# Performance work log

Hardware: AMD Instinct MI355X
Metric: run time of the kernel (lower is better)

The kernel has to match this reference:

```python
import jax, jax.numpy as jnp
import numpy as np

GROUPS = 8
EPS = 1e-5


def group_norm_dim1(x, gamma, beta):
    # Faithful to torch: GroupNorm treats dim 1 (height) as the channel axis.
    B, H, W, C = x.shape
    xg = x.reshape(B, GROUPS, H // GROUPS, W, C)
    mean = xg.mean(axis=(2, 3, 4), keepdims=True)
    var = xg.var(axis=(2, 3, 4), keepdims=True)
    xn = ((xg - mean) * jax.lax.rsqrt(var + EPS)).reshape(B, H, W, C)
    return xn * gamma[None, :, None, None] + beta[None, :, None, None]


def setup_inputs() -> dict:
    key = jax.random.key(0)
    ks = jax.random.split(key, 8)
    B, H, W, C = 4, 64, 64, 64  # height must equal units for GroupNorm to apply
    s = 1.0 / np.sqrt(C)
    return {
        "x": jax.random.normal(ks[0], (B, H, W, C), dtype=jnp.float32),
        "gamma": jnp.ones((C,), jnp.float32),
        "beta": jnp.zeros((C,), jnp.float32),
        "Wq": jax.random.normal(ks[1], (C, C), jnp.float32) * s,
        "bq": jnp.zeros((C,), jnp.float32),
        "Wk": jax.random.normal(ks[2], (C, C), jnp.float32) * s,
        "bk": jnp.zeros((C,), jnp.float32),
        "Wv": jax.random.normal(ks[3], (C, C), jnp.float32) * s,
        "bv": jnp.zeros((C,), jnp.float32),
        "Wo": jax.random.normal(ks[4], (C, C), jnp.float32) * s,
        "bo": jnp.zeros((C,), jnp.float32),
    }


def reference(x, gamma, beta, Wq, bq, Wk, bk, Wv, bv, Wo, bo):
    B, H, W, C = x.shape
    scale = C ** (-0.5)
    xn = group_norm_dim1(x, gamma, beta)
    q = xn @ Wq + bq
    k = xn @ Wk + bk
    v = xn @ Wv + bv
    # full spatial self-attention: scores [B, H, W, H*W]
    scores = jnp.einsum('bhwc,bijc->bhwij', q, k) * scale
    attn = jax.nn.softmax(scores.reshape(B, H, W, H * W), axis=-1)
    attn = attn.reshape(B, H, W, H, W)
    proj = jnp.einsum('bhwij,bijc->bhwc', attn, v)
    proj = proj @ Wo + bo
    return xn + proj
```

## Files before the change

### kernel.cpp

```cpp
#include <hip/hip_runtime.h>

typedef __bf16 bf16_t;
typedef bf16_t bf16x8 __attribute__((ext_vector_type(8)));
typedef bf16_t bf16x4 __attribute__((ext_vector_type(4)));
typedef short  short4v __attribute__((ext_vector_type(4)));
typedef float  f32x4  __attribute__((ext_vector_type(4)));

#define MFMA32(a, b, c) __builtin_amdgcn_mfma_f32_16x16x32_bf16(a, b, c, 0, 0, 0)
#define MFMA16(a, b, c) __builtin_amdgcn_mfma_f32_16x16x16bf16_1k(a, b, c, 0, 0, 0)

typedef __attribute__((address_space(3))) unsigned int       lds_u32;
typedef __attribute__((address_space(1))) const unsigned int glb_u32c;
#define DMA16(GP, LP) __builtin_amdgcn_global_load_lds((glb_u32c*)(const void*)(GP), \
                                                       (lds_u32*)(void*)(LP), 16, 0, 0)

__global__ __launch_bounds__(256) void gn1w_kernel(const float* __restrict__ x,
    float2* __restrict__ partials,
    const float* __restrict__ Wq, const float* __restrict__ Wk,
    const float* __restrict__ Wv, const float* __restrict__ Wo,
    bf16_t* __restrict__ Wt) {
  int blk = blockIdx.x, t = threadIdx.x;
  if (blk >= 256) {
    int idx = (blk - 256) * 256 + t;
    int wsel = idx >> 12, rem = idx & 4095;
    int c = rem >> 6, kk = rem & 63;
    const float* src = (wsel == 0) ? Wq : ((wsel == 1) ? Wk : ((wsel == 2) ? Wv : Wo));
    Wt[idx] = (bf16_t)src[kk * 64 + c];
    return;
  }
  const float4* x4 = (const float4*)x + (size_t)blk * 1024;
  float s = 0.f, sq = 0.f;
  #pragma unroll
  for (int u = 0; u < 4; ++u) {
    float4 v = x4[u * 256 + t];
    s  += v.x + v.y + v.z + v.w;
    sq += v.x * v.x + v.y * v.y + v.z * v.z + v.w * v.w;
  }
  for (int off = 32; off; off >>= 1) {
    s  += __shfl_down(s, off, 64);
    sq += __shfl_down(sq, off, 64);
  }
  __shared__ float2 ps[4];
  if ((t & 63) == 0) ps[t >> 6] = make_float2(s, sq);
  __syncthreads();
  if (t == 0) {
    float S = 0.f, Q = 0.f;
    #pragma unroll
    for (int i = 0; i < 4; ++i) { S += ps[i].x; Q += ps[i].y; }
    partials[blk] = make_float2(S, Q);
  }
}

__global__ __launch_bounds__(256) void gnqkv_kernel(
    const float* __restrict__ x, const float* __restrict__ gamma,
    const float* __restrict__ beta, const float2* __restrict__ parts,
    const bf16_t* __restrict__ Wt,
    const float* __restrict__ bq, const float* __restrict__ bk, const float* __restrict__ bv,
    bf16_t* __restrict__ xnb, bf16_t* __restrict__ qo, bf16_t* __restrict__ ko,
    bf16_t* __restrict__ vo) {
  __shared__ __align__(16) bf16_t xl[4096];
  int blk = blockIdx.x, t = threadIdx.x;
  int grp = blk >> 3;
  float S = 0.f, Q = 0.f;
  #pragma unroll
  for (int i = 0; i < 8; ++i) { float2 p = parts[grp * 8 + i]; S += p.x; Q += p.y; }
  float mean = S * (1.f / 32768.f);
  float rstd = rsqrtf(Q * (1.f / 32768.f) - mean * mean + 1e-5f);
  int h = blk & 63;
  float ga = gamma[h] * rstd;
  float be = beta[h] - mean * ga;
  {
    int r = t >> 2, col0 = (t & 3) * 16;
    const float4* x4 = (const float4*)(x + (size_t)blk * 4096 + r * 64 + col0);
    bf16x8 pk0, pk1;
    float4 v0 = x4[0], v1 = x4[1], v2 = x4[2], v3 = x4[3];
    pk0[0] = (bf16_t)(v0.x * ga + be); pk0[1] = (bf16_t)(v0.y * ga + be);
    pk0[2] = (bf16_t)(v0.z * ga + be); pk0[3] = (bf16_t)(v0.w * ga + be);
    pk0[4] = (bf16_t)(v1.x * ga + be); pk0[5] = (bf16_t)(v1.y * ga + be);
    pk0[6] = (bf16_t)(v1.z * ga + be); pk0[7] = (bf16_t)(v1.w * ga + be);
    pk1[0] = (bf16_t)(v2.x * ga + be); pk1[1] = (bf16_t)(v2.y * ga + be);
    pk1[2] = (bf16_t)(v2.z * ga + be); pk1[3] = (bf16_t)(v2.w * ga + be);
    pk1[4] = (bf16_t)(v3.x * ga + be); pk1[5] = (bf16_t)(v3.y * ga + be);
    pk1[6] = (bf16_t)(v3.z * ga + be); pk1[7] = (bf16_t)(v3.w * ga + be);
    *(bf16x8*)&xnb[(size_t)blk * 4096 + r * 64 + col0]     = pk0;
    *(bf16x8*)&xnb[(size_t)blk * 4096 + r * 64 + col0 + 8] = pk1;
    int sw = r & 7, j0 = (t & 3) * 2;
    *(bf16x8*)&xl[r * 64 + ((j0 ^ sw) << 3)]       = pk0;
    *(bf16x8*)&xl[r * 64 + (((j0 + 1) ^ sw) << 3)] = pk1;
  }
  __syncthreads();
  int w = t >> 6, lane = t & 63, quad = lane >> 4, l16 = lane & 15;
  int rl = w * 16 + l16, sw2 = rl & 7;
  bf16x8 a0 = *(const bf16x8*)&xl[rl * 64 + ((quad ^ sw2) << 3)];
  bf16x8 a1 = *(const bf16x8*)&xl[rl * 64 + (((quad + 4) ^ sw2) << 3)];
  int m0 = blk * 64 + w * 16;
  int bi = blk >> 6;
  int tile = blk & 63;
  size_t tbase = (size_t)bi * 262144 + (size_t)tile * 4096;
  f32x4 zero = {0.f, 0.f, 0.f, 0.f};
  const float QSCALE = 0.125f * 1.44269504088896340736f;
  #pragma unroll
  for (int outk = 0; outk < 3; ++outk) {
    const bf16_t* wt = Wt + outk * 4096;
    const float* bias = (outk == 0) ? bq : ((outk == 1) ? bk : bv);
    #pragma unroll
    for (int nt = 0; nt < 4; ++nt) {
      int col = nt * 16 + l16;
      bf16x8 b0 = *(const bf16x8*)&wt[col * 64 + quad * 8];
      bf16x8 b1 = *(const bf16x8*)&wt[col * 64 + 32 + quad * 8];
      f32x4 acc = MFMA32(a0, b0, zero);
      acc = MFMA32(a1, b1, acc);
      float bb = bias[col];
      if (outk == 0) {
        #pragma unroll
        for (int r = 0; r < 4; ++r) {
          int m = m0 + quad * 4 + r;
          qo[(size_t)m * 64 + col] = (bf16_t)((acc[r] + bb) * QSCALE);
        }
      } else if (outk == 1) {
        #pragma unroll
        for (int r = 0; r < 4; ++r) {
          int kk = (m0 & 63) + quad * 4 + r;
          ko[tbase + kk * 64 + ((((col >> 3) ^ (kk & 7)) << 3) | (col & 7))]
              = (bf16_t)(acc[r] + bb);
        }
      } else {
        bf16x4 pk;
        #pragma unroll
        for (int r = 0; r < 4; ++r) pk[r] = (bf16_t)(acc[r] + bb);
        int u = w * 4 + quad;
        *(bf16x4*)&vo[tbase + col * 64 + ((u ^ ((col & 7) << 1)) << 2)] = pk;
      }
    }
  }
}

__global__ __launch_bounds__(256, 2) void flash_kernel(
    const bf16_t* __restrict__ q, const bf16_t* __restrict__ k,
    const bf16_t* __restrict__ vp, bf16_t* __restrict__ Opb, float* __restrict__ ml) {
  __shared__ __align__(16) bf16_t Kb[2][8192];
  __shared__ __align__(16) bf16_t Vb[2][8192];
  int t = threadIdx.x;
  int w = t >> 6, lane = t & 63, quad = lane >> 4, l16 = lane & 15;
  int b = blockIdx.x, qb = blockIdx.y, sp = blockIdx.z;
  int q0 = qb * 128 + w * 32;

  bf16x8 qf[2][2];
  {
    const bf16_t* qp = q + ((size_t)b * 4096 + q0 + l16) * 64;
    #pragma unroll
    for (int qt = 0; qt < 2; ++qt)
      #pragma unroll
      for (int hh = 0; hh < 2; ++hh)
        qf[qt][hh] = *(const bf16x8*)&qp[qt * 1024 + hh * 32 + quad * 8];
  }
  f32x4 o[2][4];
  f32x4 zero = {0.f, 0.f, 0.f, 0.f};
  #pragma unroll
  for (int qt = 0; qt < 2; ++qt)
    #pragma unroll
    for (int ct = 0; ct < 4; ++ct) o[qt][ct] = zero;
  float rs[2] = {0.f, 0.f};

  const bf16_t* kimg = k  + (size_t)b * 262144 + (size_t)sp * 65536 + w * 2048 + lane * 8;
  const bf16_t* vimg = vp + (size_t)b * 262144 + (size_t)sp * 65536 + w * 2048 + lane * 8;

  #pragma unroll
  for (int i = 0; i < 4; ++i) {
    DMA16(kimg + i * 512, &Kb[0][w * 2048 + i * 512]);
    DMA16(vimg + i * 512, &Vb[0][w * 2048 + i * 512]);
  }
  __syncthreads();

  int swk = l16 & 7;
  int swv = (l16 & 7) << 1;

  for (int it = 0; it < 8; ++it) {
    int cur = it & 1;
    if (it < 7) {
      const bf16_t* kg = kimg + (it + 1) * 8192;
      const bf16_t* vg = vimg + (it + 1) * 8192;
      int nxt = cur ^ 1;
      #pragma unroll
      for (int i = 0; i < 4; ++i) {
        DMA16(kg + i * 512, &Kb[nxt][w * 2048 + i * 512]);
        DMA16(vg + i * 512, &Vb[nxt][w * 2048 + i * 512]);
      }
    }
    #pragma unroll
    for (int kt = 0; kt < 8; ++kt) {
      const bf16_t* Kh = &Kb[cur][(kt >> 2) * 4096];
      const bf16_t* Vh = &Vb[cur][(kt >> 2) * 4096];
      int krow = ((kt & 3) * 16 + l16) * 64;
      bf16x8 kf0 = *(const bf16x8*)&Kh[krow + ((quad ^ swk) << 3)];
      bf16x8 kf1 = *(const bf16x8*)&Kh[krow + (((quad + 4) ^ swk) << 3)];
      short4v va[4];
      #pragma unroll
      for (int ct = 0; ct < 4; ++ct)
        va[ct] = *(const short4v*)&Vh[(ct * 16 + l16) * 64 + ((((kt & 3) * 4 + quad) ^ swv) << 2)];
      #pragma unroll
      for (int qt = 0; qt < 2; ++qt) {
        f32x4 st = MFMA32(kf0, qf[qt][0], zero);
        st = MFMA32(kf1, qf[qt][1], st);
        bf16x4 pb;
        float psum = 0.f;
        #pragma unroll
        for (int r = 0; r < 4; ++r) {
          float p = __builtin_amdgcn_exp2f(st[r]);
          psum += p;
          pb[r] = (bf16_t)p;
        }
        rs[qt] += psum;
        short4v pshort = __builtin_bit_cast(short4v, pb);
        #pragma unroll
        for (int ct = 0; ct < 4; ++ct)
          o[qt][ct] = MFMA16(va[ct], pshort, o[qt][ct]);
      }
    }
    __syncthreads();
  }

  #pragma unroll
  for (int qt = 0; qt < 2; ++qt) {
    rs[qt] += __shfl_xor(rs[qt], 16, 64);
    rs[qt] += __shfl_xor(rs[qt], 32, 64);
  }
  size_t rbase = (size_t)sp * 16384 + (size_t)b * 4096 + q0;
  #pragma unroll
  for (int qt = 0; qt < 2; ++qt) {
    size_t row = rbase + qt * 16 + l16;
    if (quad == 0) ml[row] = rs[qt];
    #pragma unroll
    for (int ct = 0; ct < 4; ++ct) {
      bf16x4 pk;
      #pragma unroll
      for (int r = 0; r < 4; ++r) pk[r] = (bf16_t)o[qt][ct][r];
      *(bf16x4*)&Opb[row * 64 + ct * 16 + quad * 4] = pk;
    }
  }
}

__global__ __launch_bounds__(256) void proj_kernel(
    const bf16_t* __restrict__ Opb, const float* __restrict__ ml,
    const bf16_t* __restrict__ Wt, const float* __restrict__ bo,
    const bf16_t* __restrict__ xnb, float* __restrict__ out) {
  int t = threadIdx.x, w = t >> 6, lane = t & 63, quad = lane >> 4, l16 = lane & 15;
  int r0 = blockIdx.x * 64 + w * 16;
  float acc0[8], acc1[8];
  #pragma unroll
  for (int e = 0; e < 8; ++e) { acc0[e] = 0.f; acc1[e] = 0.f; }
  float lsum = 0.f;
  #pragma unroll
  for (int s = 0; s < 4; ++s) {
    size_t rr = (size_t)s * 16384 + r0 + l16;
    bf16x8 f0 = *(const bf16x8*)&Opb[rr * 64 + quad * 8];
    bf16x8 f1 = *(const bf16x8*)&Opb[rr * 64 + 32 + quad * 8];
    #pragma unroll
    for (int e = 0; e < 8; ++e) { acc0[e] += (float)f0[e]; acc1[e] += (float)f1[e]; }
    lsum += ml[rr];
  }
  float linv = 1.f / lsum;
  bf16x8 a0, a1;
  #pragma unroll
  for (int e = 0; e < 8; ++e) {
    a0[e] = (bf16_t)(acc0[e] * linv);
    a1[e] = (bf16_t)(acc1[e] * linv);
  }
  f32x4 zero = {0.f, 0.f, 0.f, 0.f};
  const bf16_t* wt = Wt + 3 * 4096;
  #pragma unroll
  for (int nt = 0; nt < 4; ++nt) {
    int col = nt * 16 + l16;
    bf16x8 b0 = *(const bf16x8*)&wt[col * 64 + quad * 8];
    bf16x8 b1 = *(const bf16x8*)&wt[col * 64 + 32 + quad * 8];
    f32x4 acc = MFMA32(a0, b0, zero);
    acc = MFMA32(a1, b1, acc);
    float bb = bo[col];
    #pragma unroll
    for (int r = 0; r < 4; ++r) {
      size_t m = (size_t)r0 + quad * 4 + r;
      out[m * 64 + col] = acc[r] + bb + (float)xnb[m * 64 + col];
    }
  }
}

extern "C" void kernel_launch(void* const* d_in, const int* in_sizes, int n_in,
                              void* d_out, int out_size, void* d_ws, size_t ws_size,
                              hipStream_t stream) {
  const float* x     = (const float*)d_in[0];
  const float* gamma = (const float*)d_in[1];
  const float* beta  = (const float*)d_in[2];
  const float* Wq    = (const float*)d_in[3];
  const float* bq    = (const float*)d_in[4];
  const float* Wk    = (const float*)d_in[5];
  const float* bk    = (const float*)d_in[6];
  const float* Wv    = (const float*)d_in[7];
  const float* bv    = (const float*)d_in[8];
  const float* Wo    = (const float*)d_in[9];
  const float* bo    = (const float*)d_in[10];
  float* out = (float*)d_out;

  char* ws = (char*)d_ws;
  bf16_t* xnb   = (bf16_t*)(ws + 0);
  bf16_t* qb    = (bf16_t*)(ws + (2u  << 20));
  bf16_t* kb    = (bf16_t*)(ws + (4u  << 20));
  bf16_t* vb    = (bf16_t*)(ws + (6u  << 20));
  bf16_t* Opb   = (bf16_t*)(ws + (8u  << 20));
  float*  ml    = (float*)(ws + (16u << 20));
  float2* parts = (float2*)(ws + (17u << 20));
  bf16_t* Wt    = (bf16_t*)(ws + (17u << 20) + 4096);

  hipLaunchKernelGGL(gn1w_kernel,  dim3(320),       dim3(256), 0, stream, x, parts, Wq, Wk, Wv, Wo, Wt);
  hipLaunchKernelGGL(gnqkv_kernel, dim3(256),       dim3(256), 0, stream, x, gamma, beta, parts, Wt, bq, bk, bv, xnb, qb, kb, vb);
  hipLaunchKernelGGL(flash_kernel, dim3(4, 32, 4),  dim3(256), 0, stream, qb, kb, vb, Opb, ml);
  hipLaunchKernelGGL(proj_kernel,  dim3(256),       dim3(256), 0, stream, Opb, ml, Wt, bo, xnb, out);
}
```

Before: 122.3 us.

## Use 16x16x32 MFMA for PV, widen query tile, double key splits

The PV product now uses the K=32 bf16 MFMA instead of the K=16 variant. Two key tiles are processed per step, and the V layout written by the QKV kernel is permuted so 8 contiguous bf16 can be loaded per lane. Each wave now handles 64 queries (256 per block), and the key range is split 8 ways instead of 4, so each block walks half the keys. The proj kernel reduces over 8 partials and the workspace offsets move to fit the larger partial buffer. The aim is fewer MFMA instructions and better reuse of K/V fragments, at the cost of more registers per thread and more partial-output traffic.

```diff
diff --git a/kernel.cpp b/kernel.cpp
--- a/kernel.cpp
+++ b/kernel.cpp
@@ -3,11 +3,9 @@
 typedef __bf16 bf16_t;
 typedef bf16_t bf16x8 __attribute__((ext_vector_type(8)));
 typedef bf16_t bf16x4 __attribute__((ext_vector_type(4)));
-typedef short  short4v __attribute__((ext_vector_type(4)));
 typedef float  f32x4  __attribute__((ext_vector_type(4)));
 
 #define MFMA32(a, b, c) __builtin_amdgcn_mfma_f32_16x16x32_bf16(a, b, c, 0, 0, 0)
-#define MFMA16(a, b, c) __builtin_amdgcn_mfma_f32_16x16x16bf16_1k(a, b, c, 0, 0, 0)
 
 typedef __attribute__((address_space(3))) unsigned int       lds_u32;
 typedef __attribute__((address_space(1))) const unsigned int glb_u32c;
@@ -128,7 +126,7 @@
         bf16x4 pk;
         #pragma unroll
         for (int r = 0; r < 4; ++r) pk[r] = (bf16_t)(acc[r] + bb);
-        int u = w * 4 + quad;
+        int u = (w >> 1) * 8 + quad * 2 + (w & 1);
         *(bf16x4*)&vo[tbase + col * 64 + ((u ^ ((col & 7) << 1)) << 2)] = pk;
       }
     }
@@ -143,27 +141,27 @@
   int t = threadIdx.x;
   int w = t >> 6, lane = t & 63, quad = lane >> 4, l16 = lane & 15;
   int b = blockIdx.x, qb = blockIdx.y, sp = blockIdx.z;
-  int q0 = qb * 128 + w * 32;
-
-  bf16x8 qf[2][2];
+  int q0 = qb * 256 + w * 64;
+
+  bf16x8 qf[4][2];
   {
     const bf16_t* qp = q + ((size_t)b * 4096 + q0 + l16) * 64;
     #pragma unroll
-    for (int qt = 0; qt < 2; ++qt)
+    for (int qt = 0; qt < 4; ++qt)
       #pragma unroll
       for (int hh = 0; hh < 2; ++hh)
         qf[qt][hh] = *(const bf16x8*)&qp[qt * 1024 + hh * 32 + quad * 8];
   }
-  f32x4 o[2][4];
+  f32x4 o[4][4];
   f32x4 zero = {0.f, 0.f, 0.f, 0.f};
   #pragma unroll
-  for (int qt = 0; qt < 2; ++qt)
+  for (int qt = 0; qt < 4; ++qt)
     #pragma unroll
     for (int ct = 0; ct < 4; ++ct) o[qt][ct] = zero;
-  float rs[2] = {0.f, 0.f};
-
-  const bf16_t* kimg = k  + (size_t)b * 262144 + (size_t)sp * 65536 + w * 2048 + lane * 8;
-  const bf16_t* vimg = vp + (size_t)b * 262144 + (size_t)sp * 65536 + w * 2048 + lane * 8;
+  float rs[4] = {0.f, 0.f, 0.f, 0.f};
+
+  const bf16_t* kimg = k  + (size_t)b * 262144 + (size_t)sp * 32768 + w * 2048 + lane * 8;
+  const bf16_t* vimg = vp + (size_t)b * 262144 + (size_t)sp * 32768 + w * 2048 + lane * 8;
 
   #pragma unroll
   for (int i = 0; i < 4; ++i) {
@@ -175,9 +173,9 @@
   int swk = l16 & 7;
   int swv = (l16 & 7) << 1;
 
-  for (int it = 0; it < 8; ++it) {
+  for (int it = 0; it < 4; ++it) {
     int cur = it & 1;
-    if (it < 7) {
+    if (it < 3) {
       const bf16_t* kg = kimg + (it + 1) * 8192;
       const bf16_t* vg = vimg + (it + 1) * 8192;
       int nxt = cur ^ 1;
@@ -188,46 +186,54 @@
       }
     }
     #pragma unroll
-    for (int kt = 0; kt < 8; ++kt) {
-      const bf16_t* Kh = &Kb[cur][(kt >> 2) * 4096];
-      const bf16_t* Vh = &Vb[cur][(kt >> 2) * 4096];
-      int krow = ((kt & 3) * 16 + l16) * 64;
-      bf16x8 kf0 = *(const bf16x8*)&Kh[krow + ((quad ^ swk) << 3)];
-      bf16x8 kf1 = *(const bf16x8*)&Kh[krow + (((quad + 4) ^ swk) << 3)];
-      short4v va[4];
+    for (int j = 0; j < 4; ++j) {
+      const bf16_t* Kh = &Kb[cur][(j >> 1) * 4096];
+      const bf16_t* Vh = &Vb[cur][(j >> 1) * 4096];
+      int k2 = j & 1;
+      int krow_a = ((k2 * 2) * 16 + l16) * 64;
+      int krow_b = ((k2 * 2 + 1) * 16 + l16) * 64;
+      bf16x8 kf0a = *(const bf16x8*)&Kh[krow_a + ((quad ^ swk) << 3)];
+      bf16x8 kf1a = *(const bf16x8*)&Kh[krow_a + (((quad + 4) ^ swk) << 3)];
+      bf16x8 kf0b = *(const bf16x8*)&Kh[krow_b + ((quad ^ swk) << 3)];
+      bf16x8 kf1b = *(const bf16x8*)&Kh[krow_b + (((quad + 4) ^ swk) << 3)];
+      int ub = k2 * 8 + quad * 2;
+      bf16x8 va8[4];
       #pragma unroll
       for (int ct = 0; ct < 4; ++ct)
-        va[ct] = *(const short4v*)&Vh[(ct * 16 + l16) * 64 + ((((kt & 3) * 4 + quad) ^ swv) << 2)];
-      #pragma unroll
-      for (int qt = 0; qt < 2; ++qt) {
-        f32x4 st = MFMA32(kf0, qf[qt][0], zero);
-        st = MFMA32(kf1, qf[qt][1], st);
-        bf16x4 pb;
+        va8[ct] = *(const bf16x8*)&Vh[(ct * 16 + l16) * 64 + ((ub ^ swv) << 2)];
+      #pragma unroll
+      for (int qt = 0; qt < 4; ++qt) {
+        f32x4 sta = MFMA32(kf0a, qf[qt][0], zero);
+        sta = MFMA32(kf1a, qf[qt][1], sta);
+        f32x4 stb = MFMA32(kf0b, qf[qt][0], zero);
+        stb = MFMA32(kf1b, qf[qt][1], stb);
+        bf16x8 pb;
         float psum = 0.f;
         #pragma unroll
         for (int r = 0; r < 4; ++r) {
-          float p = __builtin_amdgcn_exp2f(st[r]);
-          psum += p;
-          pb[r] = (bf16_t)p;
+          float pa = __builtin_amdgcn_exp2f(sta[r]);
+          float pc = __builtin_amdgcn_exp2f(stb[r]);
+          psum += pa + pc;
+          pb[r]     = (bf16_t)pa;
+          pb[r + 4] = (bf16_t)pc;
         }
         rs[qt] += psum;
-        short4v pshort = __builtin_bit_cast(short4v, pb);
         #pragma unroll
         for (int ct = 0; ct < 4; ++ct)
-          o[qt][ct] = MFMA16(va[ct], pshort, o[qt][ct]);
+          o[qt][ct] = MFMA32(va8[ct], pb, o[qt][ct]);
       }
     }
     __syncthreads();
   }
 
   #pragma unroll
-  for (int qt = 0; qt < 2; ++qt) {
+  for (int qt = 0; qt < 4; ++qt) {
     rs[qt] += __shfl_xor(rs[qt], 16, 64);
     rs[qt] += __shfl_xor(rs[qt], 32, 64);
   }
   size_t rbase = (size_t)sp * 16384 + (size_t)b * 4096 + q0;
   #pragma unroll
-  for (int qt = 0; qt < 2; ++qt) {
+  for (int qt = 0; qt < 4; ++qt) {
     size_t row = rbase + qt * 16 + l16;
     if (quad == 0) ml[row] = rs[qt];
     #pragma unroll
@@ -251,7 +257,7 @@
   for (int e = 0; e < 8; ++e) { acc0[e] = 0.f; acc1[e] = 0.f; }
   float lsum = 0.f;
   #pragma unroll
-  for (int s = 0; s < 4; ++s) {
+  for (int s = 0; s < 8; ++s) {
     size_t rr = (size_t)s * 16384 + r0 + l16;
     bf16x8 f0 = *(const bf16x8*)&Opb[rr * 64 + quad * 8];
     bf16x8 f1 = *(const bf16x8*)&Opb[rr * 64 + 32 + quad * 8];
@@ -302,16 +308,16 @@
 
   char* ws = (char*)d_ws;
   bf16_t* xnb   = (bf16_t*)(ws + 0);
-  bf16_t* qb    = (bf16_t*)(ws + (2u  << 20));
-  bf16_t* kb    = (bf16_t*)(ws + (4u  << 20));
-  bf16_t* vb    = (bf16_t*)(ws + (6u  << 20));
+  bf16_t* qbuf  = (bf16_t*)(ws + (2u  << 20));
+  bf16_t* kbuf  = (bf16_t*)(ws + (4u  << 20));
+  bf16_t* vbuf  = (bf16_t*)(ws + (6u  << 20));
   bf16_t* Opb   = (bf16_t*)(ws + (8u  << 20));
-  float*  ml    = (float*)(ws + (16u << 20));
-  float2* parts = (float2*)(ws + (17u << 20));
-  bf16_t* Wt    = (bf16_t*)(ws + (17u << 20) + 4096);
+  float*  ml    = (float*)(ws + (24u << 20));
+  float2* parts = (float2*)(ws + (25u << 20));
+  bf16_t* Wt    = (bf16_t*)(ws + (25u << 20) + 4096);
 
   hipLaunchKernelGGL(gn1w_kernel,  dim3(320),       dim3(256), 0, stream, x, parts, Wq, Wk, Wv, Wo, Wt);
-  hipLaunchKernelGGL(gnqkv_kernel, dim3(256),       dim3(256), 0, stream, x, gamma, beta, parts, Wt, bq, bk, bv, xnb, qb, kb, vb);
-  hipLaunchKernelGGL(flash_kernel, dim3(4, 32, 4),  dim3(256), 0, stream, qb, kb, vb, Opb, ml);
+  hipLaunchKernelGGL(gnqkv_kernel, dim3(256),       dim3(256), 0, stream, x, gamma, beta, parts, Wt, bq, bk, bv, xnb, qbuf, kbuf, vbuf);
+  hipLaunchKernelGGL(flash_kernel, dim3(4, 16, 8),  dim3(256), 0, stream, qbuf, kbuf, vbuf, Opb, ml);
   hipLaunchKernelGGL(proj_kernel,  dim3(256),       dim3(256), 0, stream, Opb, ml, Wt, bo, xnb, out);
 }
```

Measured after the change: 138.5 us. 13.2% more time.
